# Performance work log

Hardware: AMD Instinct MI355X
Metric: run time of the kernel (lower is better)

Reference implementation:

```python
import jax, jax.numpy as jnp
import numpy as np
import math

B, S, D, H = 2, 2048, 1024, 16
DK = D // H


def setup_inputs() -> dict:
    key = jax.random.key(0)
    ks = jax.random.split(key, 12)
    scale = 1.0 / math.sqrt(D)
    inp = {
        "query": jax.random.normal(ks[0], (B, S, D), jnp.float32),
        "key": jax.random.normal(ks[1], (B, S, D), jnp.float32),
        "value": jax.random.normal(ks[2], (B, S, D), jnp.float32),
        # causal 0/1 mask, broadcast over heads
        "mask": jnp.broadcast_to(jnp.tril(jnp.ones((S, S), jnp.int32)), (B, 1, S, S)),
        "Wq": jax.random.normal(ks[3], (D, D), jnp.float32) * scale,
        "bq": jnp.zeros((D,), jnp.float32),
        "Wk": jax.random.normal(ks[4], (D, D), jnp.float32) * scale,
        "bk": jnp.zeros((D,), jnp.float32),
        "Wv": jax.random.normal(ks[5], (D, D), jnp.float32) * scale,
        "bv": jnp.zeros((D,), jnp.float32),
        "Wo": jax.random.normal(ks[6], (D, D), jnp.float32) * scale,
        "bo": jnp.zeros((D,), jnp.float32),
    }
    return inp


def _split_heads(x):
    # [B,S,D] -> [B,H,S,DK]
    return x.reshape(B, S, H, DK).transpose(0, 2, 1, 3)


def reference(query, key, value, mask, Wq, bq, Wk, bk, Wv, bv, Wo, bo):
    q = _split_heads(query @ Wq.T + bq)
    k = _split_heads(key @ Wk.T + bk)
    v = _split_heads(value @ Wv.T + bv)
    # scaled dot-product attention with additive mask (mask==0 -> -inf)
    scores = jnp.einsum("bhqd,bhkd->bhqk", q, k) / math.sqrt(DK)
    scores = jnp.where(mask == 0, -jnp.inf, scores)
    w = jax.nn.softmax(scores, axis=-1)
    out = jnp.einsum("bhqk,bhkd->bhqd", w, v)
    out = out.transpose(0, 2, 1, 3).reshape(B, S, D)
    return out @ Wo.T + bo
```

## Files before the change

kernel.cpp:

```cpp
#include <hip/hip_runtime.h>
#include <hip/hip_bf16.h>
#include <math.h>

#define BBATCH 2
#define SSEQ 2048
#define DMODEL 1024
#define NH 16
#define MTOT (BBATCH*SSEQ)

typedef short bfrag __attribute__((ext_vector_type(8)));
typedef float ffrag __attribute__((ext_vector_type(4)));

typedef const __attribute__((address_space(1))) unsigned int* gas_t;
typedef __attribute__((address_space(3))) unsigned int* las_t;

__device__ __forceinline__ void dl16(const void* g, void* l) {
  __builtin_amdgcn_global_load_lds((gas_t)(unsigned long long)g,
                                   (las_t)(unsigned int)(unsigned long long)l,
                                   16, 0, 0);
}

__device__ __forceinline__ void drain_vm() {
  asm volatile("s_waitcnt vmcnt(0)" ::: "memory");
}

__device__ __forceinline__ unsigned short f2bf(float f) {
  union { float f; unsigned u; } v; v.f = f;
  unsigned r = v.u + 0x7fffu + ((v.u >> 16) & 1u);
  return (unsigned short)(r >> 16);
}

__global__ __launch_bounds__(256) void convert_all_kernel(
    const float* __restrict__ q, const float* __restrict__ k, const float* __restrict__ v,
    const float* __restrict__ wq, const float* __restrict__ wk,
    const float* __restrict__ wv, const float* __restrict__ wo,
    unsigned short* __restrict__ dst)
{
  const long NIN = (long)MTOT * DMODEL;
  const long NW  = (long)DMODEL * DMODEL;
  const long total4 = (3 * NIN + 4 * NW) >> 2;
  long i4 = (long)blockIdx.x * blockDim.x + threadIdx.x;
  const long stride = (long)gridDim.x * blockDim.x;
  for (; i4 < total4; i4 += stride) {
    const long i = i4 << 2;
    const float* src; long off;
    if (i < NIN)          { src = q; off = i; }
    else if (i < 2 * NIN) { src = k; off = i - NIN; }
    else if (i < 3 * NIN) { src = v; off = i - 2 * NIN; }
    else {
      const long j = i - 3 * NIN;
      const int wsel = (int)(j >> 20);
      off = j & (NW - 1);
      src = (wsel == 0) ? wq : (wsel == 1) ? wk : (wsel == 2) ? wv : wo;
    }
    const float4 x = *(const float4*)(src + off);
    ushort4 o;
    o.x = f2bf(x.x); o.y = f2bf(x.y); o.z = f2bf(x.z); o.w = f2bf(x.w);
    *(ushort4*)(dst + i) = o;
  }
}

struct ProjArgs {
  const unsigned short* X[3];
  const unsigned short* W[3];
  const float* bias[3];
  unsigned short* dst[3];
  float scale[3];
};

__global__ __launch_bounds__(256, 2) void qkv_proj(ProjArgs a)
{
  __shared__ alignas(16) unsigned short As[128 * 64];
  __shared__ alignas(16) unsigned short Bs[128 * 64];
  const int t = threadIdx.x;
  const int lane = t & 63, w = t >> 6;
  const int quad = lane >> 4, l16 = lane & 15;
  const int m0 = blockIdx.x * 128;
  const int n0 = blockIdx.y * 128;
  const int z = blockIdx.z;
  const unsigned short* __restrict__ X = a.X[z];
  const unsigned short* __restrict__ W = a.W[z];
  const int wm = (w & 1) * 64, wn = (w >> 1) * 64;

  ffrag acc[4][4];
#pragma unroll
  for (int i = 0; i < 4; ++i)
#pragma unroll
    for (int j = 0; j < 4; ++j)
#pragma unroll
      for (int e = 0; e < 4; ++e) acc[i][j][e] = 0.f;

  for (int kk = 0; kk < 16; ++kk) {
    const int k0 = kk * 64;
    __syncthreads();
#pragma unroll
    for (int i = 0; i < 4; ++i) {
      const int ch = i * 256 + t;
      const int row = ch >> 3, pc = ch & 7;
      dl16(X + (size_t)(m0 + row) * DMODEL + k0 + pc * 8, As + ch * 8);
      dl16(W + (size_t)(n0 + row) * DMODEL + k0 + pc * 8, Bs + ch * 8);
    }
    drain_vm();
    __syncthreads();

    bfrag af[4][2], bg[4][2];
#pragma unroll
    for (int fi = 0; fi < 4; ++fi)
#pragma unroll
      for (int c = 0; c < 2; ++c) {
        af[fi][c] = *(const bfrag*)&As[(wm + fi * 16 + l16) * 64 + c * 32 + quad * 8];
        bg[fi][c] = *(const bfrag*)&Bs[(wn + fi * 16 + l16) * 64 + c * 32 + quad * 8];
      }
#pragma unroll
    for (int c = 0; c < 2; ++c)
#pragma unroll
      for (int fi = 0; fi < 4; ++fi)
#pragma unroll
        for (int fj = 0; fj < 4; ++fj)
          acc[fi][fj] = __builtin_amdgcn_mfma_f32_16x16x32_bf16(af[fi][c], bg[fj][c], acc[fi][fj], 0, 0, 0);
  }

  const float sc = a.scale[z];
  const float* __restrict__ bias = a.bias[z];
  unsigned short* __restrict__ dst = a.dst[z];
#pragma unroll
  for (int fj = 0; fj < 4; ++fj) {
    const int n = n0 + wn + fj * 16 + l16;
    const float bv = bias[n];
    const int h = n >> 6, dk = n & 63;
    if (z < 2) {
#pragma unroll
      for (int fi = 0; fi < 4; ++fi)
#pragma unroll
        for (int r = 0; r < 4; ++r) {
          const int m = m0 + wm + fi * 16 + quad * 4 + r;
          const int b_ = m >> 11, s_ = m & (SSEQ - 1);
          dst[((size_t)(b_ * NH + h) * SSEQ + s_) * 64 + dk] = f2bf((acc[fi][fj][r] + bv) * sc);
        }
    } else {
#pragma unroll
      for (int fi = 0; fi < 4; ++fi) {
        const int m = m0 + wm + fi * 16 + quad * 4;
        const int b_ = m >> 11, s_ = m & (SSEQ - 1);
        ushort4 pk;
        pk.x = f2bf(acc[fi][fj][0] + bv);
        pk.y = f2bf(acc[fi][fj][1] + bv);
        pk.z = f2bf(acc[fi][fj][2] + bv);
        pk.w = f2bf(acc[fi][fj][3] + bv);
        *(ushort4*)&dst[((size_t)(b_ * NH + h) * 64 + dk) * SSEQ + s_] = pk;
      }
    }
  }
}

__global__ __launch_bounds__(256, 2) void out_proj(
    const unsigned short* __restrict__ X,
    const unsigned short* __restrict__ W,
    const float* __restrict__ bias,
    float* __restrict__ Y)
{
  __shared__ alignas(16) unsigned short As[128 * 64];
  __shared__ alignas(16) unsigned short Bs[128 * 64];
  const int t = threadIdx.x;
  const int lane = t & 63, w = t >> 6;
  const int quad = lane >> 4, l16 = lane & 15;
  const int m0 = blockIdx.x * 128;
  const int n0 = blockIdx.y * 128;
  const int wm = (w & 1) * 64, wn = (w >> 1) * 64;

  ffrag acc[4][4];
#pragma unroll
  for (int i = 0; i < 4; ++i)
#pragma unroll
    for (int j = 0; j < 4; ++j)
#pragma unroll
      for (int e = 0; e < 4; ++e) acc[i][j][e] = 0.f;

  for (int kk = 0; kk < 16; ++kk) {
    const int k0 = kk * 64;
    __syncthreads();
#pragma unroll
    for (int i = 0; i < 4; ++i) {
      const int ch = i * 256 + t;
      const int row = ch >> 3, pc = ch & 7;
      dl16(X + (size_t)(m0 + row) * DMODEL + k0 + pc * 8, As + ch * 8);
      dl16(W + (size_t)(n0 + row) * DMODEL + k0 + pc * 8, Bs + ch * 8);
    }
    drain_vm();
    __syncthreads();

    bfrag af[4][2], bg[4][2];
#pragma unroll
    for (int fi = 0; fi < 4; ++fi)
#pragma unroll
      for (int c = 0; c < 2; ++c) {
        af[fi][c] = *(const bfrag*)&As[(wm + fi * 16 + l16) * 64 + c * 32 + quad * 8];
        bg[fi][c] = *(const bfrag*)&Bs[(wn + fi * 16 + l16) * 64 + c * 32 + quad * 8];
      }
#pragma unroll
    for (int c = 0; c < 2; ++c)
#pragma unroll
      for (int fi = 0; fi < 4; ++fi)
#pragma unroll
        for (int fj = 0; fj < 4; ++fj)
          acc[fi][fj] = __builtin_amdgcn_mfma_f32_16x16x32_bf16(af[fi][c], bg[fj][c], acc[fi][fj], 0, 0, 0);
  }

#pragma unroll
  for (int fj = 0; fj < 4; ++fj) {
    const int n = n0 + wn + fj * 16 + l16;
    const float bv = bias[n];
#pragma unroll
    for (int fi = 0; fi < 4; ++fi)
#pragma unroll
      for (int r = 0; r < 4; ++r) {
        const int m = m0 + wm + fi * 16 + quad * 4 + r;
        Y[(size_t)m * DMODEL + n] = acc[fi][fj][r] + bv;
      }
  }
}

__global__ __launch_bounds__(256, 4) void attn_mfma(
    const unsigned short* __restrict__ Q,
    const unsigned short* __restrict__ K,
    const unsigned short* __restrict__ Vt_g,
    unsigned short* __restrict__ ctx)
{
  __shared__ alignas(16) unsigned short Kb[2][64 * 64];
  __shared__ alignas(16) unsigned short Vb[2][64 * 64];
  __shared__ alignas(16) unsigned short Pt[4][16 * 64];

  const int t = threadIdx.x;
  const int lane = t & 63, w = t >> 6;
  const int quad = lane >> 4, l16 = lane & 15;
  const int bh = blockIdx.y;
  const int qtile = blockIdx.z ? (31 - (int)blockIdx.x) : (int)blockIdx.x;
  const int i0 = qtile * 64;
  const int b_ = bh >> 4, h_ = bh & (NH - 1);
  const int q_l = w * 16 + l16;

  const unsigned short* kg = K + (size_t)bh * SSEQ * 64;
  const unsigned short* vg = Vt_g + (size_t)bh * 64 * SSEQ;

  int koff[2], voff[2], loff[2];
#pragma unroll
  for (int i = 0; i < 2; ++i) {
    const int ch = i * 256 + t;
    const int r = ch >> 3;
    const int lc = (ch & 7) ^ (r & 7);
    koff[i] = r * 64 + lc * 8;
    voff[i] = r * SSEQ + lc * 8;
    loff[i] = ch * 8;
  }
  int sw[2];
#pragma unroll
  for (int c = 0; c < 2; ++c) sw[c] = (((c * 4 + quad) ^ (l16 & 7)) * 8);
  const int pwr = l16 * 64 + (quad & 1) * 4;

  const unsigned short* qg = Q + ((size_t)bh * SSEQ + i0) * 64;

#pragma unroll
  for (int i = 0; i < 2; ++i) {
    dl16(kg + koff[i], Kb[0] + loff[i]);
    dl16(vg + voff[i], Vb[0] + loff[i]);
  }

  bfrag qb[2];
#pragma unroll
  for (int c = 0; c < 2; ++c)
    qb[c] = *(const bfrag*)(qg + (size_t)q_l * 64 + c * 32 + quad * 8);

  ffrag o[4];
#pragma unroll
  for (int fn = 0; fn < 4; ++fn)
#pragma unroll
    for (int e = 0; e < 4; ++e) o[fn][e] = 0.f;
  float lsum = 0.f;

  for (int jt = 0; jt <= qtile; ++jt) {
    const int cur = jt & 1;
    drain_vm();
    __syncthreads();

    if (jt < qtile) {
      const int nxt = cur ^ 1;
#pragma unroll
      for (int i = 0; i < 2; ++i) {
        dl16(kg + (size_t)(jt + 1) * 4096 + koff[i], Kb[nxt] + loff[i]);
        dl16(vg + (size_t)(jt + 1) * 64   + voff[i], Vb[nxt] + loff[i]);
      }
    }

    ffrag s[4];
#pragma unroll
    for (int fj = 0; fj < 4; ++fj)
#pragma unroll
      for (int e = 0; e < 4; ++e) s[fj][e] = 0.f;
#pragma unroll
    for (int c = 0; c < 2; ++c)
#pragma unroll
      for (int fj = 0; fj < 4; ++fj) {
        bfrag ka = *(const bfrag*)&Kb[cur][(fj * 16 + l16) * 64 + sw[c]];
        s[fj] = __builtin_amdgcn_mfma_f32_16x16x32_bf16(ka, qb[c], s[fj], 0, 0, 0);
      }

    const bool diag = (jt == qtile);
#pragma unroll
    for (int fj = 0; fj < 4; ++fj) {
      float p[4];
#pragma unroll
      for (int r = 0; r < 4; ++r) {
        float pe = exp2f(s[fj][r]);
        if (diag && (fj * 16 + quad * 4 + r) > q_l) pe = 0.f;
        p[r] = pe;
        lsum += pe;
      }
      float2 lo; lo.x = p[0]; lo.y = p[1];
      float2 hi; hi.x = p[2]; hi.y = p[3];
      union { __hip_bfloat162 h[2]; unsigned long long u; } cv;
      cv.h[0] = __float22bfloat162_rn(lo);
      cv.h[1] = __float22bfloat162_rn(hi);
      const int cc = fj * 2 + (quad >> 1);
      *(unsigned long long*)&Pt[w][pwr + ((cc ^ (l16 & 7)) * 8)] = cv.u;
    }
    asm volatile("s_waitcnt lgkmcnt(0)" ::: "memory");

#pragma unroll
    for (int c = 0; c < 2; ++c) {
      bfrag pb = *(const bfrag*)&Pt[w][l16 * 64 + sw[c]];
#pragma unroll
      for (int fn = 0; fn < 4; ++fn) {
        bfrag va = *(const bfrag*)&Vb[cur][(fn * 16 + l16) * 64 + sw[c]];
        o[fn] = __builtin_amdgcn_mfma_f32_16x16x32_bf16(va, pb, o[fn], 0, 0, 0);
      }
    }
  }

  lsum += __shfl_xor(lsum, 16);
  lsum += __shfl_xor(lsum, 32);

  const float inv = 1.f / lsum;
  unsigned short* cbase = ctx + (size_t)(b_ * SSEQ + i0 + q_l) * DMODEL + h_ * 64;
#pragma unroll
  for (int fn = 0; fn < 4; ++fn) {
    float2 lo; lo.x = o[fn][0] * inv; lo.y = o[fn][1] * inv;
    float2 hi; hi.x = o[fn][2] * inv; hi.y = o[fn][3] * inv;
    union { __hip_bfloat162 h[2]; unsigned long long u; } cv;
    cv.h[0] = __float22bfloat162_rn(lo);
    cv.h[1] = __float22bfloat162_rn(hi);
    *(unsigned long long*)(cbase + fn * 16 + quad * 4) = cv.u;
  }
}

extern "C" void kernel_launch(void* const* d_in, const int* in_sizes, int n_in,
                              void* d_out, int out_size, void* d_ws, size_t ws_size,
                              hipStream_t stream)
{
  const float* q  = (const float*)d_in[0];
  const float* k  = (const float*)d_in[1];
  const float* v  = (const float*)d_in[2];
  const float* wq = (const float*)d_in[4];
  const float* bq = (const float*)d_in[5];
  const float* wk = (const float*)d_in[6];
  const float* bk = (const float*)d_in[7];
  const float* wv = (const float*)d_in[8];
  const float* bv = (const float*)d_in[9];
  const float* wo = (const float*)d_in[10];
  const float* bo = (const float*)d_in[11];

  const long NIN = (long)MTOT * DMODEL;
  const long NW  = (long)DMODEL * DMODEL;
  unsigned short* ws16 = (unsigned short*)d_ws;
  unsigned short* qx  = ws16;
  unsigned short* kx  = qx + NIN;
  unsigned short* vx  = kx + NIN;
  unsigned short* wqb = vx + NIN;
  unsigned short* wkb = wqb + NW;
  unsigned short* wvb = wkb + NW;
  unsigned short* wob = wvb + NW;
  unsigned short* Qp  = wob + NW;
  unsigned short* Kp  = Qp + NIN;
  unsigned short* Vp  = Kp + NIN;
  unsigned short* Cx  = Vp + NIN;

  convert_all_kernel<<<2048, 256, 0, stream>>>(q, k, v, wq, wk, wv, wo, ws16);

  ProjArgs pa;
  pa.X[0] = qx;  pa.X[1] = kx;  pa.X[2] = vx;
  pa.W[0] = wqb; pa.W[1] = wkb; pa.W[2] = wvb;
  pa.bias[0] = bq; pa.bias[1] = bk; pa.bias[2] = bv;
  pa.dst[0] = Qp; pa.dst[1] = Kp; pa.dst[2] = Vp;
  pa.scale[0] = 0.18033688011112042f;
  pa.scale[1] = 1.0f;
  pa.scale[2] = 1.0f;
  qkv_proj<<<dim3(MTOT / 128, DMODEL / 128, 3), 256, 0, stream>>>(pa);

  attn_mfma<<<dim3(16, BBATCH * NH, 2), 256, 0, stream>>>(Qp, Kp, Vp, Cx);

  out_proj<<<dim3(MTOT / 128, DMODEL / 128), 256, 0, stream>>>(Cx, wob, bo, (float*)d_out);
}
```

Baseline: 238.4 us.

## Double-buffer GEMM tiles, widen convert loads, enlarge attention query tile

```diff
diff --git a/kernel.cpp b/kernel.cpp
--- a/kernel.cpp
+++ b/kernel.cpp
@@ -38,11 +38,11 @@
 {
   const long NIN = (long)MTOT * DMODEL;
   const long NW  = (long)DMODEL * DMODEL;
-  const long total4 = (3 * NIN + 4 * NW) >> 2;
-  long i4 = (long)blockIdx.x * blockDim.x + threadIdx.x;
+  const long total8 = (3 * NIN + 4 * NW) >> 3;
+  long i8 = (long)blockIdx.x * blockDim.x + threadIdx.x;
   const long stride = (long)gridDim.x * blockDim.x;
-  for (; i4 < total4; i4 += stride) {
-    const long i = i4 << 2;
+  for (; i8 < total8; i8 += stride) {
+    const long i = i8 << 3;
     const float* src; long off;
     if (i < NIN)          { src = q; off = i; }
     else if (i < 2 * NIN) { src = k; off = i - NIN; }
@@ -53,10 +53,13 @@
       off = j & (NW - 1);
       src = (wsel == 0) ? wq : (wsel == 1) ? wk : (wsel == 2) ? wv : wo;
     }
-    const float4 x = *(const float4*)(src + off);
-    ushort4 o;
-    o.x = f2bf(x.x); o.y = f2bf(x.y); o.z = f2bf(x.z); o.w = f2bf(x.w);
-    *(ushort4*)(dst + i) = o;
+    const float4 x0 = *(const float4*)(src + off);
+    const float4 x1 = *(const float4*)(src + off + 4);
+    ushort4 o0, o1;
+    o0.x = f2bf(x0.x); o0.y = f2bf(x0.y); o0.z = f2bf(x0.z); o0.w = f2bf(x0.w);
+    o1.x = f2bf(x1.x); o1.y = f2bf(x1.y); o1.z = f2bf(x1.z); o1.w = f2bf(x1.w);
+    union { ushort4 s[2]; uint4 u; } pk; pk.s[0] = o0; pk.s[1] = o1;
+    *(uint4*)(dst + i) = pk.u;
   }
 }
 
@@ -70,8 +73,8 @@
 
 __global__ __launch_bounds__(256, 2) void qkv_proj(ProjArgs a)
 {
-  __shared__ alignas(16) unsigned short As[128 * 64];
-  __shared__ alignas(16) unsigned short Bs[128 * 64];
+  __shared__ alignas(16) unsigned short As[2][128 * 64];
+  __shared__ alignas(16) unsigned short Bs[2][128 * 64];
   const int t = threadIdx.x;
   const int lane = t & 63, w = t >> 6;
   const int quad = lane >> 4, l16 = lane & 15;
@@ -90,26 +93,37 @@
 #pragma unroll
       for (int e = 0; e < 4; ++e) acc[i][j][e] = 0.f;
 
+#pragma unroll
+  for (int i = 0; i < 4; ++i) {
+    const int ch = i * 256 + t;
+    const int row = ch >> 3, pc = ch & 7;
+    dl16(X + (size_t)(m0 + row) * DMODEL + pc * 8, As[0] + ch * 8);
+    dl16(W + (size_t)(n0 + row) * DMODEL + pc * 8, Bs[0] + ch * 8);
+  }
+
   for (int kk = 0; kk < 16; ++kk) {
-    const int k0 = kk * 64;
-    __syncthreads();
-#pragma unroll
-    for (int i = 0; i < 4; ++i) {
-      const int ch = i * 256 + t;
-      const int row = ch >> 3, pc = ch & 7;
-      dl16(X + (size_t)(m0 + row) * DMODEL + k0 + pc * 8, As + ch * 8);
-      dl16(W + (size_t)(n0 + row) * DMODEL + k0 + pc * 8, Bs + ch * 8);
-    }
+    const int cur = kk & 1;
     drain_vm();
     __syncthreads();
 
+    if (kk < 15) {
+      const int k1 = (kk + 1) * 64, nxt = cur ^ 1;
+#pragma unroll
+      for (int i = 0; i < 4; ++i) {
+        const int ch = i * 256 + t;
+        const int row = ch >> 3, pc = ch & 7;
+        dl16(X + (size_t)(m0 + row) * DMODEL + k1 + pc * 8, As[nxt] + ch * 8);
+        dl16(W + (size_t)(n0 + row) * DMODEL + k1 + pc * 8, Bs[nxt] + ch * 8);
+      }
+    }
+
     bfrag af[4][2], bg[4][2];
 #pragma unroll
     for (int fi = 0; fi < 4; ++fi)
 #pragma unroll
       for (int c = 0; c < 2; ++c) {
-        af[fi][c] = *(const bfrag*)&As[(wm + fi * 16 + l16) * 64 + c * 32 + quad * 8];
-        bg[fi][c] = *(const bfrag*)&Bs[(wn + fi * 16 + l16) * 64 + c * 32 + quad * 8];
+        af[fi][c] = *(const bfrag*)&As[cur][(wm + fi * 16 + l16) * 64 + c * 32 + quad * 8];
+        bg[fi][c] = *(const bfrag*)&Bs[cur][(wn + fi * 16 + l16) * 64 + c * 32 + quad * 8];
       }
 #pragma unroll
     for (int c = 0; c < 2; ++c)
@@ -159,55 +173,75 @@
     const float* __restrict__ bias,
     float* __restrict__ Y)
 {
-  __shared__ alignas(16) unsigned short As[128 * 64];
-  __shared__ alignas(16) unsigned short Bs[128 * 64];
+  __shared__ alignas(16) unsigned short As[2][128 * 64];
+  __shared__ alignas(16) unsigned short Bs[2][64 * 64];
   const int t = threadIdx.x;
   const int lane = t & 63, w = t >> 6;
   const int quad = lane >> 4, l16 = lane & 15;
   const int m0 = blockIdx.x * 128;
-  const int n0 = blockIdx.y * 128;
-  const int wm = (w & 1) * 64, wn = (w >> 1) * 64;
-
-  ffrag acc[4][4];
+  const int n0 = blockIdx.y * 64;
+  const int wm = (w & 1) * 64, wn = (w >> 1) * 32;
+
+  ffrag acc[4][2];
 #pragma unroll
   for (int i = 0; i < 4; ++i)
 #pragma unroll
-    for (int j = 0; j < 4; ++j)
+    for (int j = 0; j < 2; ++j)
 #pragma unroll
       for (int e = 0; e < 4; ++e) acc[i][j][e] = 0.f;
 
+#pragma unroll
+  for (int i = 0; i < 4; ++i) {
+    const int ch = i * 256 + t;
+    dl16(X + (size_t)(m0 + (ch >> 3)) * DMODEL + (ch & 7) * 8, As[0] + ch * 8);
+  }
+#pragma unroll
+  for (int i = 0; i < 2; ++i) {
+    const int ch = i * 256 + t;
+    dl16(W + (size_t)(n0 + (ch >> 3)) * DMODEL + (ch & 7) * 8, Bs[0] + ch * 8);
+  }
+
   for (int kk = 0; kk < 16; ++kk) {
-    const int k0 = kk * 64;
-    __syncthreads();
-#pragma unroll
-    for (int i = 0; i < 4; ++i) {
-      const int ch = i * 256 + t;
-      const int row = ch >> 3, pc = ch & 7;
-      dl16(X + (size_t)(m0 + row) * DMODEL + k0 + pc * 8, As + ch * 8);
-      dl16(W + (size_t)(n0 + row) * DMODEL + k0 + pc * 8, Bs + ch * 8);
-    }
+    const int cur = kk & 1;
     drain_vm();
     __syncthreads();
 
-    bfrag af[4][2], bg[4][2];
+    if (kk < 15) {
+      const int k1 = (kk + 1) * 64, nxt = cur ^ 1;
+#pragma unroll
+      for (int i = 0; i < 4; ++i) {
+        const int ch = i * 256 + t;
+        dl16(X + (size_t)(m0 + (ch >> 3)) * DMODEL + k1 + (ch & 7) * 8, As[nxt] + ch * 8);
+      }
+#pragma unroll
+      for (int i = 0; i < 2; ++i) {
+        const int ch = i * 256 + t;
+        dl16(W + (size_t)(n0 + (ch >> 3)) * DMODEL + k1 + (ch & 7) * 8, Bs[nxt] + ch * 8);
+      }
+    }
+
+    bfrag af[4][2], bg[2][2];
 #pragma unroll
     for (int fi = 0; fi < 4; ++fi)
 #pragma unroll
-      for (int c = 0; c < 2; ++c) {
-        af[fi][c] = *(const bfrag*)&As[(wm + fi * 16 + l16) * 64 + c * 32 + quad * 8];
-        bg[fi][c] = *(const bfrag*)&Bs[(wn + fi * 16 + l16) * 64 + c * 32 + quad * 8];
-      }
+      for (int c = 0; c < 2; ++c)
+        af[fi][c] = *(const bfrag*)&As[cur][(wm + fi * 16 + l16) * 64 + c * 32 + quad * 8];
+#pragma unroll
+    for (int fj = 0; fj < 2; ++fj)
+#pragma unroll
+      for (int c = 0; c < 2; ++c)
+        bg[fj][c] = *(const bfrag*)&Bs[cur][(wn + fj * 16 + l16) * 64 + c * 32 + quad * 8];
 #pragma unroll
     for (int c = 0; c < 2; ++c)
 #pragma unroll
       for (int fi = 0; fi < 4; ++fi)
 #pragma unroll
-        for (int fj = 0; fj < 4; ++fj)
+        for (int fj = 0; fj < 2; ++fj)
           acc[fi][fj] = __builtin_amdgcn_mfma_f32_16x16x32_bf16(af[fi][c], bg[fj][c], acc[fi][fj], 0, 0, 0);
   }
 
 #pragma unroll
-  for (int fj = 0; fj < 4; ++fj) {
+  for (int fj = 0; fj < 2; ++fj) {
     const int n = n0 + wn + fj * 16 + l16;
     const float bv = bias[n];
 #pragma unroll
@@ -220,7 +254,7 @@
   }
 }
 
-__global__ __launch_bounds__(256, 4) void attn_mfma(
+__global__ __launch_bounds__(512, 4) void attn_mfma(
     const unsigned short* __restrict__ Q,
     const unsigned short* __restrict__ K,
     const unsigned short* __restrict__ Vt_g,
@@ -228,43 +262,36 @@
 {
   __shared__ alignas(16) unsigned short Kb[2][64 * 64];
   __shared__ alignas(16) unsigned short Vb[2][64 * 64];
-  __shared__ alignas(16) unsigned short Pt[4][16 * 64];
+  __shared__ alignas(16) unsigned short Pt[8][16 * 64];
 
   const int t = threadIdx.x;
   const int lane = t & 63, w = t >> 6;
   const int quad = lane >> 4, l16 = lane & 15;
   const int bh = blockIdx.y;
-  const int qtile = blockIdx.z ? (31 - (int)blockIdx.x) : (int)blockIdx.x;
-  const int i0 = qtile * 64;
+  const int Xt = blockIdx.z ? (15 - (int)blockIdx.x) : (int)blockIdx.x;
+  const int i0 = Xt * 128;
+  const int jtmax = 2 * Xt + 1;
   const int b_ = bh >> 4, h_ = bh & (NH - 1);
   const int q_l = w * 16 + l16;
 
   const unsigned short* kg = K + (size_t)bh * SSEQ * 64;
   const unsigned short* vg = Vt_g + (size_t)bh * 64 * SSEQ;
 
-  int koff[2], voff[2], loff[2];
-#pragma unroll
-  for (int i = 0; i < 2; ++i) {
-    const int ch = i * 256 + t;
-    const int r = ch >> 3;
-    const int lc = (ch & 7) ^ (r & 7);
-    koff[i] = r * 64 + lc * 8;
-    voff[i] = r * SSEQ + lc * 8;
-    loff[i] = ch * 8;
-  }
+  const int r_ = t >> 3;
+  const int lc = (t & 7) ^ (r_ & 7);
+  const int koff = r_ * 64 + lc * 8;
+  const int voff = r_ * SSEQ + lc * 8;
+  const int loff = t * 8;
+
   int sw[2];
 #pragma unroll
   for (int c = 0; c < 2; ++c) sw[c] = (((c * 4 + quad) ^ (l16 & 7)) * 8);
   const int pwr = l16 * 64 + (quad & 1) * 4;
 
+  dl16(kg + koff, Kb[0] + loff);
+  dl16(vg + voff, Vb[0] + loff);
+
   const unsigned short* qg = Q + ((size_t)bh * SSEQ + i0) * 64;
-
-#pragma unroll
-  for (int i = 0; i < 2; ++i) {
-    dl16(kg + koff[i], Kb[0] + loff[i]);
-    dl16(vg + voff[i], Vb[0] + loff[i]);
-  }
-
   bfrag qb[2];
 #pragma unroll
   for (int c = 0; c < 2; ++c)
@@ -277,18 +304,15 @@
     for (int e = 0; e < 4; ++e) o[fn][e] = 0.f;
   float lsum = 0.f;
 
-  for (int jt = 0; jt <= qtile; ++jt) {
+  for (int jt = 0; jt <= jtmax; ++jt) {
     const int cur = jt & 1;
     drain_vm();
     __syncthreads();
 
-    if (jt < qtile) {
+    if (jt < jtmax) {
       const int nxt = cur ^ 1;
-#pragma unroll
-      for (int i = 0; i < 2; ++i) {
-        dl16(kg + (size_t)(jt + 1) * 4096 + koff[i], Kb[nxt] + loff[i]);
-        dl16(vg + (size_t)(jt + 1) * 64   + voff[i], Vb[nxt] + loff[i]);
-      }
+      dl16(kg + (size_t)(jt + 1) * 4096 + koff, Kb[nxt] + loff);
+      dl16(vg + (size_t)(jt + 1) * 64   + voff, Vb[nxt] + loff);
     }
 
     ffrag s[4];
@@ -304,14 +328,15 @@
         s[fj] = __builtin_amdgcn_mfma_f32_16x16x32_bf16(ka, qb[c], s[fj], 0, 0, 0);
       }
 
-    const bool diag = (jt == qtile);
+    const int kbase = (jt - 2 * Xt) * 64;
+    const bool diag = (kbase >= 0);
 #pragma unroll
     for (int fj = 0; fj < 4; ++fj) {
       float p[4];
 #pragma unroll
       for (int r = 0; r < 4; ++r) {
         float pe = exp2f(s[fj][r]);
-        if (diag && (fj * 16 + quad * 4 + r) > q_l) pe = 0.f;
+        if (diag && (kbase + fj * 16 + quad * 4 + r) > q_l) pe = 0.f;
         p[r] = pe;
         lsum += pe;
       }
@@ -395,7 +420,7 @@
   pa.scale[2] = 1.0f;
   qkv_proj<<<dim3(MTOT / 128, DMODEL / 128, 3), 256, 0, stream>>>(pa);
 
-  attn_mfma<<<dim3(16, BBATCH * NH, 2), 256, 0, stream>>>(Qp, Kp, Vp, Cx);
-
-  out_proj<<<dim3(MTOT / 128, DMODEL / 128), 256, 0, stream>>>(Cx, wob, bo, (float*)d_out);
-}
+  attn_mfma<<<dim3(8, BBATCH * NH, 2), 512, 0, stream>>>(Qp, Kp, Vp, Cx);
+
+  out_proj<<<dim3(MTOT / 128, DMODEL / 64), 256, 0, stream>>>(Cx, wob, bo, (float*)d_out);
+}
```

Measured after the change: 243.6 us. 1.02x slower.
